# Optimization experiments

Hardware: AMD Instinct MI355X
Metric: run time of the kernel (lower is better)

## Reference

```python
import jax, jax.numpy as jnp
import numpy as np

B, H, W, C = 32, 56, 56, 192
WS, SS, NH = 7, 3, 6  # window, shift, heads
N = WS * WS
HIDDEN = int(C * 4.0)
TABLE = (2 * WS - 1) * (2 * WS - 1)  # 169
EPS = 1e-5

# Relative position index, faithful to the source (meshgrid default 'xy',
# and the source multiplies BOTH coord channels by (2*ws-1), so indices can
# exceed the table size; gather uses clip like jnp.take's jit behavior).
_coords = np.stack(np.meshgrid(np.arange(WS), np.arange(WS))).reshape(2, -1)
_rel = (_coords[:, :, None] - _coords[:, None, :]).transpose(1, 2, 0)
_rel = (_rel + WS - 1) * (2 * WS - 1)
REL_IDX = jnp.asarray(_rel.sum(-1))  # [N, N]

# Shift attention mask (static), labels regions then marks cross-region pairs.
_m = np.zeros((H, W))
_cnt = 0
for hs in [slice(0, -WS), slice(-WS, -SS), slice(-SS, None)]:
    for ws_ in [slice(0, -WS), slice(-WS, -SS), slice(-SS, None)]:
        _m[hs, ws_] = _cnt
        _cnt += 1
_mw = _m.reshape(H // WS, WS, W // WS, WS).transpose(0, 2, 1, 3).reshape(-1, N)
ATTN_MASK = jnp.asarray((_mw[:, None, :] != _mw[:, :, None]).astype(np.float32))  # [nW, N, N]
NW = ATTN_MASK.shape[0]


def layer_norm(x, g, b):
    mu = jnp.mean(x, axis=-1, keepdims=True)
    xc = x - mu
    var = jnp.mean(xc * xc, axis=-1, keepdims=True)
    return xc * jax.lax.rsqrt(var + EPS) * g + b


def window_partition(x):  # [B,H,W,C] -> [B*nW, N, C]
    x = x.reshape(B, H // WS, WS, W // WS, WS, C).transpose(0, 1, 3, 2, 4, 5)
    return x.reshape(-1, N, C)


def window_reverse(w):  # [B*nW, N, C] -> [B,H,W,C]
    x = w.reshape(B, H // WS, W // WS, WS, WS, C).transpose(0, 1, 3, 2, 4, 5)
    return x.reshape(B, H, W, C)


def setup_inputs() -> dict:
    key = jax.random.key(0)
    ks = jax.random.split(key, 16)
    s = lambda fan_in: 1.0 / np.sqrt(fan_in)
    return {
        "x": jax.random.normal(ks[0], (B, H * W, C), jnp.float32),
        "norm1_g": jnp.ones((C,), jnp.float32),
        "norm1_b": jnp.zeros((C,), jnp.float32),
        "qkv_w": jax.random.normal(ks[1], (C, 3 * C), jnp.float32) * s(C),
        "qkv_b": jnp.zeros((3 * C,), jnp.float32),
        "rel_table": jax.random.normal(ks[2], (TABLE, NH), jnp.float32) * 0.02,
        "proj_w": jax.random.normal(ks[3], (C, C), jnp.float32) * s(C),
        "proj_b": jnp.zeros((C,), jnp.float32),
        "norm2_g": jnp.ones((C,), jnp.float32),
        "norm2_b": jnp.zeros((C,), jnp.float32),
        "fc1_w": jax.random.normal(ks[4], (C, HIDDEN), jnp.float32) * s(C),
        "fc1_b": jnp.zeros((HIDDEN,), jnp.float32),
        "fc2_w": jax.random.normal(ks[5], (HIDDEN, C), jnp.float32) * s(HIDDEN),
        "fc2_b": jnp.zeros((C,), jnp.float32),
    }


def reference(x, norm1_g, norm1_b, qkv_w, qkv_b, rel_table, proj_w, proj_b,
              norm2_g, norm2_b, fc1_w, fc1_b, fc2_w, fc2_b):
    shortcut = x
    h = layer_norm(x, norm1_g, norm1_b).reshape(B, H, W, C)
    # cyclic shift
    h = jnp.roll(h, shift=(-SS, -SS), axis=(1, 2))
    xw = window_partition(h)  # [B*nW, N, C]

    # window attention
    qkv = xw @ qkv_w + qkv_b  # [B*nW, N, 3C]
    q, k, v = jnp.split(qkv, 3, axis=-1)
    hd = C // NH
    q = q.reshape(-1, N, NH, hd).transpose(0, 2, 1, 3) * (hd ** -0.5)
    k = k.reshape(-1, N, NH, hd).transpose(0, 2, 1, 3)
    v = v.reshape(-1, N, NH, hd).transpose(0, 2, 1, 3)
    attn = jnp.einsum("whnd,whmd->whnm", q, k)  # [B*nW, NH, N, N]
    bias = jnp.take(rel_table, REL_IDX, axis=0, mode="clip")  # [N,N,NH]
    attn = attn + bias.transpose(2, 0, 1)[None]
    attn = attn.reshape(B, NW, NH, N, N) + ATTN_MASK[None, :, None] * -100.0
    attn = jax.nn.softmax(attn.reshape(-1, NH, N, N), axis=-1)
    o = jnp.einsum("whnm,whmd->whnd", attn, v)
    o = o.transpose(0, 2, 1, 3).reshape(-1, N, C)
    o = o @ proj_w + proj_b

    h = window_reverse(o)
    h = jnp.roll(h, shift=(SS, SS), axis=(1, 2)).reshape(B, H * W, C)
    x = shortcut + h
    # MLP
    m = layer_norm(x, norm2_g, norm2_b)
    m = jax.nn.gelu(m @ fc1_w + fc1_b, approximate=False) @ fc2_w + fc2_b
    return x + m
```

## Files before the change

### kernel.cpp

```cpp
#include <hip/hip_runtime.h>
#include <hip/hip_bf16.h>


using f32x4  = __attribute__((ext_vector_type(4))) float;
using short8 = __attribute__((ext_vector_type(8))) short;
typedef unsigned short ushort_t;

__device__ __forceinline__ ushort_t f2bf(float f) {
    __hip_bfloat16 h = __float2bfloat16(f);
    return __builtin_bit_cast(ushort_t, h);
}
__device__ __forceinline__ f32x4 mfma16(short8 a, short8 b, f32x4 c) {
    return __builtin_amdgcn_mfma_f32_16x16x32_bf16(a, b, c, 0, 0, 0);
}
__device__ __forceinline__ float fast_gelu(float h) {
    float hh = h * h;
    float p  = __builtin_fmaf(hh, 0.044715f, 1.0f);
    float z  = h * (-1.5957691216057308f);
    float em = __expf(p * z);
    return h * __builtin_amdgcn_rcpf(1.0f + em);
}

#define CC 192

#define OFF_QKVT   0
#define OFF_PROJT  221184
#define OFF_FC1T   294912
#define OFF_FC2T   589824
#define OFF_BIAS   884736
#define OFF_MASK   942592
#define OFF_BMT    1557504
#define OFF_QG     7848960
#define OFF_KG     46384128
#define OFF_VG     84919296
#define WS_NEED    123454464
#define PREP_SMALL 610438
#define PREP_BIG   2183302

__global__ void prep_kernel(const float* __restrict__ qkv_w, const float* __restrict__ proj_w,
                            const float* __restrict__ fc1_w, const float* __restrict__ fc2_w,
                            const float* __restrict__ rel_table,
                            ushort_t* __restrict__ qkvT, ushort_t* __restrict__ projT,
                            ushort_t* __restrict__ fc1T, ushort_t* __restrict__ fc2T,
                            float* __restrict__ biasT, float* __restrict__ maskT,
                            float* __restrict__ bmT, int full) {
    int idx = blockIdx.x * 256 + threadIdx.x;
    if (idx < 110592) { int n = idx / 192, k = idx % 192; qkvT[idx] = f2bf(qkv_w[k * 576 + n]); return; }
    idx -= 110592;
    if (idx < 36864) { int n = idx / 192, k = idx % 192; projT[idx] = f2bf(proj_w[k * 192 + n]); return; }
    idx -= 36864;
    if (idx < 147456) { int n = idx / 192, k = idx % 192; fc1T[idx] = f2bf(fc1_w[k * 768 + n]); return; }
    idx -= 147456;
    if (idx < 147456) { int n = idx / 768, k = idx % 768; fc2T[idx] = f2bf(fc2_w[k * 192 + n]); return; }
    idx -= 147456;
    if (idx < 14406) {
        int h = idx / 2401; int rest = idx % 2401; int a = rest / 49, b = rest % 49;
        int d = 13 * ((a % 7) - (b % 7) + (a / 7) - (b / 7) + 12);
        if (d > 168) d = 168;
        biasT[idx] = rel_table[d * 6 + h];
        return;
    }
    idx -= 14406;
    if (idx < 153664) {
        int w = idx / 2401; int rest = idx % 2401; int a = rest / 49, b = rest % 49;
        int wy = w / 8, wx = w % 8;
        int ya = wy * 7 + a / 7, xa = wx * 7 + a % 7;
        int yb = wy * 7 + b / 7, xb = wx * 7 + b % 7;
        int lya = ya < 49 ? 0 : (ya < 53 ? 1 : 2);
        int lxa = xa < 49 ? 0 : (xa < 53 ? 1 : 2);
        int lyb = yb < 49 ? 0 : (yb < 53 ? 1 : 2);
        int lxb = xb < 49 ? 0 : (xb < 53 ? 1 : 2);
        maskT[idx] = ((lya * 3 + lxa) != (lyb * 3 + lxb)) ? -100.0f : 0.0f;
        return;
    }
    idx -= 153664;
    if (full && idx < 1572864) {
        int wi = idx / 24576; int r2 = idx % 24576;
        int h = r2 / 4096; int r3 = r2 % 4096;
        int col = r3 / 64, row = r3 % 64;
        float v = -1e30f;
        if (row < 49 && col < 49) {
            int d = 13 * ((row % 7) - (col % 7) + (row / 7) - (col / 7) + 12);
            if (d > 168) d = 168;
            float bias = rel_table[d * 6 + h];
            int wy = wi / 8, wx = wi % 8;
            int ya = wy * 7 + row / 7, xa = wx * 7 + row % 7;
            int yb = wy * 7 + col / 7, xb = wx * 7 + col % 7;
            int lya = ya < 49 ? 0 : (ya < 53 ? 1 : 2);
            int lxa = xa < 49 ? 0 : (xa < 53 ? 1 : 2);
            int lyb = yb < 49 ? 0 : (yb < 53 ? 1 : 2);
            int lxb = xb < 49 ? 0 : (xb < 53 ? 1 : 2);
            float mask = ((lya * 3 + lxa) != (lyb * 3 + lxb)) ? -100.0f : 0.0f;
            v = bias + mask;
        }
        bmT[idx] = v;
        return;
    }
}

__global__ __launch_bounds__(256, 3) void lnqkv_kernel(
    const float* __restrict__ x, const float* __restrict__ n1g, const float* __restrict__ n1b,
    const ushort_t* __restrict__ qkvT, const float* __restrict__ qkv_b,
    ushort_t* __restrict__ qg, ushort_t* __restrict__ kg, ushort_t* __restrict__ vg) {
    __shared__ ushort_t xln [64 * 200];
    __shared__ ushort_t qkvs[64 * 200];
    const int tid = threadIdx.x;
    const int wave = tid >> 6, lane = tid & 63;
    const int ln16 = lane & 15, sub = lane >> 4;
    const int t0 = blockIdx.x * 64;
    const f32x4 zero4 = {0.f, 0.f, 0.f, 0.f};

    {
        float g0 = n1g[lane], g1 = n1g[lane + 64], g2 = n1g[lane + 128];
        float bb0 = n1b[lane], bb1 = n1b[lane + 64], bb2 = n1b[lane + 128];
        for (int rb = 0; rb < 4; ++rb) {
            int row0 = wave * 16 + rb * 4;
            float v0[4], v1[4], v2[4], s[4], q[4];
            #pragma unroll
            for (int j = 0; j < 4; ++j) {
                const float* xr = x + (size_t)(t0 + row0 + j) * CC;
                v0[j] = xr[lane]; v1[j] = xr[lane + 64]; v2[j] = xr[lane + 128];
            }
            #pragma unroll
            for (int j = 0; j < 4; ++j) {
                s[j] = v0[j] + v1[j] + v2[j];
                q[j] = v0[j] * v0[j] + v1[j] * v1[j] + v2[j] * v2[j];
            }
            #pragma unroll
            for (int m = 32; m; m >>= 1) {
                #pragma unroll
                for (int j = 0; j < 4; ++j) { s[j] += __shfl_xor(s[j], m); q[j] += __shfl_xor(q[j], m); }
            }
            #pragma unroll
            for (int j = 0; j < 4; ++j) {
                float mu = s[j] * (1.0f / 192.0f);
                float var = q[j] * (1.0f / 192.0f) - mu * mu;
                float rs = rsqrtf(var + 1e-5f);
                int row = row0 + j;
                xln[row * 200 + lane]       = f2bf((v0[j] - mu) * rs * g0 + bb0);
                xln[row * 200 + lane + 64]  = f2bf((v1[j] - mu) * rs * g1 + bb1);
                xln[row * 200 + lane + 128] = f2bf((v2[j] - mu) * rs * g2 + bb2);
            }
        }
    }
    __syncthreads();

    ushort_t* dsts[3] = {qg, kg, vg};
    for (int v = 0; v < 3; ++v) {
        f32x4 acc[4][3];
        #pragma unroll
        for (int m = 0; m < 4; ++m)
            #pragma unroll
            for (int n = 0; n < 3; ++n) acc[m][n] = zero4;
        for (int kk = 0; kk < 6; ++kk) {
            short8 a[4];
            #pragma unroll
            for (int m = 0; m < 4; ++m)
                a[m] = *(const short8*)(xln + (m * 16 + ln16) * 200 + kk * 32 + 8 * sub);
            #pragma unroll
            for (int n = 0; n < 3; ++n) {
                short8 b = *(const short8*)(qkvT + (size_t)(v * 192 + (wave * 3 + n) * 16 + ln16) * 192 + kk * 32 + 8 * sub);
                #pragma unroll
                for (int m = 0; m < 4; ++m) acc[m][n] = mfma16(a[m], b, acc[m][n]);
            }
        }
        #pragma unroll
        for (int n = 0; n < 3; ++n) {
            int col = (wave * 3 + n) * 16 + ln16;
            float bv = qkv_b[v * 192 + col];
            #pragma unroll
            for (int m = 0; m < 4; ++m)
                #pragma unroll
                for (int r = 0; r < 4; ++r) {
                    int row = m * 16 + 4 * sub + r;
                    float val = acc[m][n][r] + bv;
                    if (v == 0) val *= 0.17677669529663689f;
                    qkvs[row * 200 + col] = f2bf(val);
                }
        }
        __syncthreads();
        ushort_t* dst = dsts[v];
        for (int i = tid; i < 1536; i += 256) {
            int row = i / 24, c = i % 24;
            short8 vv = *(const short8*)(qkvs + row * 200 + c * 8);
            *(short8*)(dst + (size_t)(t0 + row) * 192 + c * 8) = vv;
        }
        __syncthreads();
    }
}

__global__ __launch_bounds__(256, 3) void attnmlp_kernel(
    const float* __restrict__ x, const float* __restrict__ proj_b,
    const ushort_t* __restrict__ qg, const ushort_t* __restrict__ kg,
    const ushort_t* __restrict__ vg, const ushort_t* __restrict__ projT,
    const float* __restrict__ bmT,
    const float* __restrict__ n2g, const float* __restrict__ n2b,
    const float* __restrict__ fc1_b, const float* __restrict__ fc2_b,
    const ushort_t* __restrict__ fc1T, const ushort_t* __restrict__ fc2T,
    float* __restrict__ out) {
    __shared__ __align__(16) char smem[51200];
    ushort_t* vt   = (ushort_t*)smem;
    ushort_t* PO   = (ushort_t*)(smem + 27648);
    ushort_t* aln  = (ushort_t*)smem;
    ushort_t* hidc = (ushort_t*)(smem + 25600);
    float*    fout = (float*)smem;

    const int tid = threadIdx.x;
    const int wave = tid >> 6, lane = tid & 63;
    const int ln16 = lane & 15, sub = lane >> 4;
    const int win = blockIdx.x;
    const int b = win >> 6, wi = win & 63;
    const int wy = wi >> 3, wx = wi & 7;
    const f32x4 zero4 = {0.f, 0.f, 0.f, 0.f};

    size_t tokA;
    {
        int j = wave * 16 + ln16; if (j > 48) j = 48;
        int y  = wy * 7 + j / 7 + 3; if (y >= 56) y -= 56;
        int xx = wx * 7 + j % 7 + 3; if (xx >= 56) xx -= 56;
        tokA = (size_t)(b * 3136 + y * 56 + xx);
    }
    size_t tokB[4];
    #pragma unroll
    for (int n = 0; n < 4; ++n) {
        int j = n * 16 + ln16; if (j > 48) j = 48;
        int y  = wy * 7 + j / 7 + 3; if (y >= 56) y -= 56;
        int xx = wx * 7 + j % 7 + 3; if (xx >= 56) xx -= 56;
        tokB[n] = (size_t)(b * 3136 + y * 56 + xx);
    }
    const float* bmw = bmT + (size_t)wi * 24576 + (size_t)(wave * 16 + 4 * sub);

    short8 qf = *(const short8*)(qg + tokA * 192 + 8 * sub);
    short8 kf[4];
    f32x4  bv[4];
    #pragma unroll
    for (int n = 0; n < 4; ++n) {
        kf[n] = *(const short8*)(kg + tokB[n] * 192 + 8 * sub);
        bv[n] = *(const f32x4*)(bmw + (n * 16 + ln16) * 64);
    }

    {
        int j = tid & 63;
        int jj = j < 49 ? j : 48;
        int y  = wy * 7 + jj / 7 + 3; if (y >= 56) y -= 56;
        int xx = wx * 7 + jj % 7 + 3; if (xx >= 56) xx -= 56;
        size_t tokV = (size_t)(b * 3136 + y * 56 + xx);
        const bool valid = j < 49;
        #pragma unroll
        for (int pass = 0; pass < 6; ++pass) {
            int c8 = pass * 32 + (tid >> 6) * 8;
            if (valid) {
                short8 vv = *(const short8*)(vg + tokV * 192 + c8);
                #pragma unroll
                for (int q = 0; q < 8; ++q) vt[(c8 + q) * 72 + j] = ((ushort_t*)&vv)[q];
            } else {
                #pragma unroll
                for (int q = 0; q < 8; ++q) vt[(c8 + q) * 72 + j] = 0;
            }
        }
    }

    f32x4 accP[12];
    #pragma unroll
    for (int n = 0; n < 12; ++n) accP[n] = zero4;
    ushort_t* Pw = PO + wave * (16 * 72);
    __syncthreads();

    #pragma unroll
    for (int h = 0; h < 6; ++h) {
        f32x4 s4[4];
        #pragma unroll
        for (int n = 0; n < 4; ++n) s4[n] = mfma16(qf, kf[n], zero4);
        short8 qn; short8 kn[4]; f32x4 bn[4];
        if (h < 5) {
            qn = *(const short8*)(qg + tokA * 192 + (h + 1) * 32 + 8 * sub);
            #pragma unroll
            for (int n = 0; n < 4; ++n) {
                kn[n] = *(const short8*)(kg + tokB[n] * 192 + (h + 1) * 32 + 8 * sub);
                bn[n] = *(const f32x4*)(bmw + (h + 1) * 4096 + (n * 16 + ln16) * 64);
            }
        }
        #pragma unroll
        for (int n = 0; n < 4; ++n)
            #pragma unroll
            for (int r = 0; r < 4; ++r) s4[n][r] += bv[n][r];
        #pragma unroll
        for (int r = 0; r < 4; ++r) {
            float mx = fmaxf(fmaxf(s4[0][r], s4[1][r]), fmaxf(s4[2][r], s4[3][r]));
            mx = fmaxf(mx, __shfl_xor(mx, 1, 16));
            mx = fmaxf(mx, __shfl_xor(mx, 2, 16));
            mx = fmaxf(mx, __shfl_xor(mx, 4, 16));
            mx = fmaxf(mx, __shfl_xor(mx, 8, 16));
            float e0 = __expf(s4[0][r] - mx), e1 = __expf(s4[1][r] - mx);
            float e2 = __expf(s4[2][r] - mx), e3 = __expf(s4[3][r] - mx);
            float sm = e0 + e1 + e2 + e3;
            sm += __shfl_xor(sm, 1, 16);
            sm += __shfl_xor(sm, 2, 16);
            sm += __shfl_xor(sm, 4, 16);
            sm += __shfl_xor(sm, 8, 16);
            float inv = 1.0f / sm;
            int rl = 4 * sub + r;
            Pw[rl * 72 +      ln16] = f2bf(e0 * inv);
            Pw[rl * 72 + 16 + ln16] = f2bf(e1 * inv);
            Pw[rl * 72 + 32 + ln16] = f2bf(e2 * inv);
            Pw[rl * 72 + 48 + ln16] = f2bf(e3 * inv);
        }
        short8 ap0 = *(const short8*)(Pw + ln16 * 72 + 8 * sub);
        short8 ap1 = *(const short8*)(Pw + ln16 * 72 + 32 + 8 * sub);
        f32x4 o2[2]; o2[0] = zero4; o2[1] = zero4;
        #pragma unroll
        for (int n2 = 0; n2 < 2; ++n2) {
            short8 bv0 = *(const short8*)(vt + (h * 32 + n2 * 16 + ln16) * 72 + 8 * sub);
            short8 bv1 = *(const short8*)(vt + (h * 32 + n2 * 16 + ln16) * 72 + 32 + 8 * sub);
            o2[n2] = mfma16(ap0, bv0, o2[n2]);
            o2[n2] = mfma16(ap1, bv1, o2[n2]);
        }
        #pragma unroll
        for (int n2 = 0; n2 < 2; ++n2)
            #pragma unroll
            for (int r = 0; r < 4; ++r)
                Pw[(4 * sub + r) * 72 + n2 * 16 + ln16] = f2bf(o2[n2][r]);
        {
            short8 ao = *(const short8*)(Pw + ln16 * 72 + 8 * sub);
            #pragma unroll
            for (int n = 0; n < 12; ++n) {
                short8 bp = *(const short8*)(projT + (size_t)(n * 16 + ln16) * 192 + h * 32 + 8 * sub);
                accP[n] = mfma16(ao, bp, accP[n]);
            }
        }
        if (h < 5) {
            qf = qn;
            #pragma unroll
            for (int n = 0; n < 4; ++n) { kf[n] = kn[n]; bv[n] = bn[n]; }
        }
    }

    #pragma unroll
    for (int n = 0; n < 12; ++n) {
        int col = n * 16 + ln16;
        float pb = proj_b[col];
        #pragma unroll
        for (int r = 0; r < 4; ++r) {
            int row = wave * 16 + 4 * sub + r;
            float v = accP[n][r] + pb;
            if (row < 49) {
                int y  = wy * 7 + row / 7 + 3; if (y >= 56) y -= 56;
                int xx = wx * 7 + row % 7 + 3; if (xx >= 56) xx -= 56;
                size_t g = (size_t)(b * 3136 + y * 56 + xx) * CC;
                v += x[g + col];
                out[g + col] = v;
            }
            accP[n][r] = v;
        }
    }
    __threadfence_block();

    float mu4[4], rs4[4];
    {
        float s[4], qs[4];
        #pragma unroll
        for (int r = 0; r < 4; ++r) { s[r] = 0.f; qs[r] = 0.f; }
        #pragma unroll
        for (int n = 0; n < 12; ++n)
            #pragma unroll
            for (int r = 0; r < 4; ++r) {
                float v = accP[n][r];
                s[r] += v; qs[r] += v * v;
            }
        #pragma unroll
        for (int m = 1; m < 16; m <<= 1) {
            #pragma unroll
            for (int r = 0; r < 4; ++r) {
                s[r]  += __shfl_xor(s[r],  m, 16);
                qs[r] += __shfl_xor(qs[r], m, 16);
            }
        }
        #pragma unroll
        for (int r = 0; r < 4; ++r) {
            float mu = s[r] * (1.0f / 192.0f);
            float var = qs[r] * (1.0f / 192.0f) - mu * mu;
            mu4[r] = mu;
            rs4[r] = rsqrtf(var + 1e-5f);
        }
    }
    __syncthreads();

    short8 b1p[3];
    #pragma unroll
    for (int n = 0; n < 3; ++n)
        b1p[n] = *(const short8*)(fc1T + (size_t)(wave * 48 + n * 16 + ln16) * 192 + 8 * sub);

    #pragma unroll
    for (int n = 0; n < 12; ++n) {
        int col = n * 16 + ln16;
        float g = n2g[col], bb = n2b[col];
        #pragma unroll
        for (int r = 0; r < 4; ++r) {
            int row = wave * 16 + 4 * sub + r;
            aln[row * 200 + col] = f2bf((accP[n][r] - mu4[r]) * rs4[r] * g + bb);
        }
    }
    __syncthreads();

    f32x4 accO[4][3];
    #pragma unroll
    for (int m = 0; m < 4; ++m)
        #pragma unroll
        for (int n = 0; n < 3; ++n) accO[m][n] = zero4;

    for (int c = 0; c < 4; ++c) {
        f32x4 acc1[4][3];
        #pragma unroll
        for (int m = 0; m < 4; ++m)
            #pragma unroll
            for (int n = 0; n < 3; ++n) acc1[m][n] = zero4;
        #pragma unroll
        for (int kk = 0; kk < 6; ++kk) {
            short8 a[4];
            #pragma unroll
            for (int m = 0; m < 4; ++m)
                a[m] = *(const short8*)(aln + (m * 16 + ln16) * 200 + kk * 32 + 8 * sub);
            short8 bb[3];
            if (kk == 0) {
                bb[0] = b1p[0]; bb[1] = b1p[1]; bb[2] = b1p[2];
            } else {
                #pragma unroll
                for (int n = 0; n < 3; ++n)
                    bb[n] = *(const short8*)(fc1T + (size_t)(c * 192 + wave * 48 + n * 16 + ln16) * 192 + kk * 32 + 8 * sub);
            }
            __builtin_amdgcn_s_setprio(1);
            #pragma unroll
            for (int n = 0; n < 3; ++n)
                #pragma unroll
                for (int m = 0; m < 4; ++m) acc1[m][n] = mfma16(a[m], bb[n], acc1[m][n]);
            __builtin_amdgcn_s_setprio(0);
        }
        short8 b2p[3];
        #pragma unroll
        for (int n = 0; n < 3; ++n)
            b2p[n] = *(const short8*)(fc2T + (size_t)(wave * 48 + n * 16 + ln16) * 768 + c * 192 + 8 * sub);
        if (c < 3) {
            #pragma unroll
            for (int n = 0; n < 3; ++n)
                b1p[n] = *(const short8*)(fc1T + (size_t)((c + 1) * 192 + wave * 48 + n * 16 + ln16) * 192 + 8 * sub);
        }
        #pragma unroll
        for (int n = 0; n < 3; ++n) {
            int cl = wave * 48 + n * 16 + ln16;
            float fb = fc1_b[c * 192 + cl];
            #pragma unroll
            for (int m = 0; m < 4; ++m)
                #pragma unroll
                for (int r = 0; r < 4; ++r) {
                    float hv = acc1[m][n][r] + fb;
                    hidc[(m * 16 + 4 * sub + r) * 200 + cl] = f2bf(fast_gelu(hv));
                }
        }
        __syncthreads();
        #pragma unroll
        for (int kk = 0; kk < 6; ++kk) {
            short8 a[4];
            #pragma unroll
            for (int m = 0; m < 4; ++m)
                a[m] = *(const short8*)(hidc + (m * 16 + ln16) * 200 + kk * 32 + 8 * sub);
            short8 bb[3];
            if (kk == 0) {
                bb[0] = b2p[0]; bb[1] = b2p[1]; bb[2] = b2p[2];
            } else {
                #pragma unroll
                for (int n = 0; n < 3; ++n)
                    bb[n] = *(const short8*)(fc2T + (size_t)(wave * 48 + n * 16 + ln16) * 768 + c * 192 + kk * 32 + 8 * sub);
            }
            __builtin_amdgcn_s_setprio(1);
            #pragma unroll
            for (int n = 0; n < 3; ++n)
                #pragma unroll
                for (int m = 0; m < 4; ++m) accO[m][n] = mfma16(a[m], bb[n], accO[m][n]);
            __builtin_amdgcn_s_setprio(0);
        }
        __syncthreads();
    }

    #pragma unroll
    for (int n = 0; n < 3; ++n) {
        int col = wave * 48 + n * 16 + ln16;
        float fb = fc2_b[col];
        #pragma unroll
        for (int m = 0; m < 4; ++m)
            #pragma unroll
            for (int r = 0; r < 4; ++r)
                fout[(m * 16 + 4 * sub + r) * 196 + col] = accO[m][n][r] + fb;
    }
    __syncthreads();
    for (int i = tid; i < 2352; i += 256) {
        int row = i / 48, c4 = (i % 48) * 4;
        int y  = wy * 7 + row / 7 + 3; if (y >= 56) y -= 56;
        int xx = wx * 7 + row % 7 + 3; if (xx >= 56) xx -= 56;
        float* op = out + (size_t)(b * 3136 + y * 56 + xx) * CC + c4;
        f32x4 sv = *(const f32x4*)(fout + row * 196 + c4);
        f32x4 ov = *(const f32x4*)op;
        #pragma unroll
        for (int q = 0; q < 4; ++q) ov[q] += sv[q];
        *(f32x4*)op = ov;
    }
}

__global__ __launch_bounds__(256, 3) void attn_kernel(
    const float* __restrict__ x, const float* __restrict__ n1g, const float* __restrict__ n1b,
    const float* __restrict__ qkv_b, const float* __restrict__ proj_b,
    const ushort_t* __restrict__ qkvT, const ushort_t* __restrict__ projT,
    const float* __restrict__ biasT, const float* __restrict__ maskT,
    float* __restrict__ out) {
    __shared__ ushort_t xln[64 * 200];
    __shared__ ushort_t qo [64 * 40];
    __shared__ ushort_t kl [64 * 40];
    __shared__ ushort_t vt [32 * 72];
    __shared__ ushort_t Pl [64 * 72];
    const int tid = threadIdx.x;
    const int wave = tid >> 6, lane = tid & 63;
    const int ln16 = lane & 15, sub = lane >> 4;
    const int w = blockIdx.x;
    const int batch = w >> 6, wi = w & 63;
    const int wy = wi >> 3, wx = wi & 7;
    const f32x4 zero4 = {0.f, 0.f, 0.f, 0.f};

    for (int rr = 0; rr < 16; ++rr) {
        int row = wave * 16 + rr;
        if (row < 49) {
            int ty = row / 7, tx = row % 7;
            int y  = wy * 7 + ty + 3; if (y >= 56) y -= 56;
            int xx = wx * 7 + tx + 3; if (xx >= 56) xx -= 56;
            const float* xr = x + (size_t)(batch * 3136 + y * 56 + xx) * CC;
            float v0 = xr[lane], v1 = xr[lane + 64], v2 = xr[lane + 128];
            float s = v0 + v1 + v2;
            #pragma unroll
            for (int m = 32; m; m >>= 1) s += __shfl_xor(s, m);
            float mu = s * (1.0f / 192.0f);
            float d0 = v0 - mu, d1 = v1 - mu, d2 = v2 - mu;
            float q = d0 * d0 + d1 * d1 + d2 * d2;
            #pragma unroll
            for (int m = 32; m; m >>= 1) q += __shfl_xor(q, m);
            float rs = rsqrtf(q * (1.0f / 192.0f) + 1e-5f);
            xln[row * 200 + lane]       = f2bf(d0 * rs * n1g[lane]       + n1b[lane]);
            xln[row * 200 + lane + 64]  = f2bf(d1 * rs * n1g[lane + 64]  + n1b[lane + 64]);
            xln[row * 200 + lane + 128] = f2bf(d2 * rs * n1g[lane + 128] + n1b[lane + 128]);
        } else {
            xln[row * 200 + lane] = 0; xln[row * 200 + lane + 64] = 0; xln[row * 200 + lane + 128] = 0;
        }
    }

    f32x4 accP[12];
    #pragma unroll
    for (int n = 0; n < 12; ++n) accP[n] = zero4;
    const float scale = 0.17677669529663689f;
    const float* mptr = maskT + wi * 2401;

    for (int h = 0; h < 6; ++h) {
        f32x4 acc6[6];
        #pragma unroll
        for (int n = 0; n < 6; ++n) acc6[n] = zero4;
        const int cb0 = h * 32;
        for (int kk = 0; kk < 6; ++kk) {
            short8 a = *(const short8*)(xln + (wave * 16 + ln16) * 200 + kk * 32 + 8 * sub);
            #pragma unroll
            for (int n = 0; n < 6; ++n) {
                int colbase = (n >> 1) * 192 + cb0 + (n & 1) * 16;
                short8 b = *(const short8*)(qkvT + (size_t)(colbase + ln16) * 192 + kk * 32 + 8 * sub);
                acc6[n] = mfma16(a, b, acc6[n]);
            }
        }
        #pragma unroll
        for (int n = 0; n < 6; ++n) {
            int colbase = (n >> 1) * 192 + cb0 + (n & 1) * 16;
            float bv = qkv_b[colbase + ln16];
            int dim = (n & 1) * 16 + ln16;
            #pragma unroll
            for (int r = 0; r < 4; ++r) {
                int row = wave * 16 + 4 * sub + r;
                ushort_t hv = f2bf(acc6[n][r] + bv);
                if (n < 2)      qo[row * 40 + dim] = hv;
                else if (n < 4) kl[row * 40 + dim] = hv;
                else            vt[dim * 72 + row] = hv;
            }
        }
        __syncthreads();

        f32x4 s4[4];
        {
            short8 aq = *(const short8*)(qo + (wave * 16 + ln16) * 40 + 8 * sub);
            #pragma unroll
            for (int n = 0; n < 4; ++n) {
                short8 bk = *(const short8*)(kl + (n * 16 + ln16) * 40 + 8 * sub);
                s4[n] = mfma16(aq, bk, zero4);
            }
        }
        const float* bptr = biasT + h * 2401;
        #pragma unroll
        for (int n = 0; n < 4; ++n) {
            int col = n * 16 + ln16;
            #pragma unroll
            for (int r = 0; r < 4; ++r) {
                int row = wave * 16 + 4 * sub + r;
                s4[n][r] = (row < 49 && col < 49)
                    ? s4[n][r] * scale + bptr[row * 49 + col] + mptr[row * 49 + col]
                    : -1e30f;
            }
        }
        #pragma unroll
        for (int r = 0; r < 4; ++r) {
            float mx = fmaxf(fmaxf(s4[0][r], s4[1][r]), fmaxf(s4[2][r], s4[3][r]));
            mx = fmaxf(mx, __shfl_xor(mx, 1, 16));
            mx = fmaxf(mx, __shfl_xor(mx, 2, 16));
            mx = fmaxf(mx, __shfl_xor(mx, 4, 16));
            mx = fmaxf(mx, __shfl_xor(mx, 8, 16));
            float e0 = __expf(s4[0][r] - mx), e1 = __expf(s4[1][r] - mx);
            float e2 = __expf(s4[2][r] - mx), e3 = __expf(s4[3][r] - mx);
            float sm = e0 + e1 + e2 + e3;
            sm += __shfl_xor(sm, 1, 16);
            sm += __shfl_xor(sm, 2, 16);
            sm += __shfl_xor(sm, 4, 16);
            sm += __shfl_xor(sm, 8, 16);
            float inv = 1.0f / sm;
            int row = wave * 16 + 4 * sub + r;
            Pl[row * 72 +      ln16] = f2bf(e0 * inv);
            Pl[row * 72 + 16 + ln16] = f2bf(e1 * inv);
            Pl[row * 72 + 32 + ln16] = f2bf(e2 * inv);
            Pl[row * 72 + 48 + ln16] = f2bf(e3 * inv);
        }
        f32x4 o2[2]; o2[0] = zero4; o2[1] = zero4;
        #pragma unroll
        for (int ks = 0; ks < 2; ++ks) {
            short8 ap = *(const short8*)(Pl + (wave * 16 + ln16) * 72 + ks * 32 + 8 * sub);
            #pragma unroll
            for (int n2 = 0; n2 < 2; ++n2) {
                short8 bv = *(const short8*)(vt + (n2 * 16 + ln16) * 72 + ks * 32 + 8 * sub);
                o2[n2] = mfma16(ap, bv, o2[n2]);
            }
        }
        #pragma unroll
        for (int n2 = 0; n2 < 2; ++n2)
            #pragma unroll
            for (int r = 0; r < 4; ++r) {
                int row = wave * 16 + 4 * sub + r;
                qo[row * 40 + n2 * 16 + ln16] = f2bf(o2[n2][r]);
            }
        {
            short8 ao = *(const short8*)(qo + (wave * 16 + ln16) * 40 + 8 * sub);
            #pragma unroll
            for (int n = 0; n < 12; ++n) {
                short8 bp = *(const short8*)(projT + (size_t)(n * 16 + ln16) * 192 + h * 32 + 8 * sub);
                accP[n] = mfma16(ao, bp, accP[n]);
            }
        }
        __syncthreads();
    }

    #pragma unroll
    for (int n = 0; n < 12; ++n) {
        int col = n * 16 + ln16;
        float pb = proj_b[col];
        #pragma unroll
        for (int r = 0; r < 4; ++r) {
            int row = wave * 16 + 4 * sub + r;
            if (row < 49) {
                int ty = row / 7, tx = row % 7;
                int y  = wy * 7 + ty + 3; if (y >= 56) y -= 56;
                int xx = wx * 7 + tx + 3; if (xx >= 56) xx -= 56;
                size_t g = (size_t)(batch * 3136 + y * 56 + xx) * CC;
                out[g + col] = accP[n][r] + pb + x[g + col];
            }
        }
    }
}

__global__ __launch_bounds__(256, 3) void mlp5_kernel(
    float* __restrict__ out, const float* __restrict__ n2g, const float* __restrict__ n2b,
    const float* __restrict__ fc1_b, const float* __restrict__ fc2_b,
    const ushort_t* __restrict__ fc1T, const ushort_t* __restrict__ fc2T) {
    __shared__ ushort_t smem[2][64 * 200];
    ushort_t* aln  = smem[0];
    ushort_t* hidc = smem[1];
    float* fout = (float*)&smem[0][0];
    const int tid = threadIdx.x;
    const int wave = tid >> 6, lane = tid & 63;
    const int ln16 = lane & 15, sub = lane >> 4;
    const size_t t0 = (size_t)blockIdx.x * 64;
    const f32x4 zero4 = {0.f, 0.f, 0.f, 0.f};

    short8 b1p[3];
    #pragma unroll
    for (int n = 0; n < 3; ++n)
        b1p[n] = *(const short8*)(fc1T + (size_t)(wave * 48 + n * 16 + ln16) * 192 + 8 * sub);

    {
        float g0 = n2g[lane], g1 = n2g[lane + 64], g2 = n2g[lane + 128];
        float bb0 = n2b[lane], bb1 = n2b[lane + 64], bb2 = n2b[lane + 128];
        for (int rb = 0; rb < 4; ++rb) {
            int row0 = wave * 16 + rb * 4;
            float v0[4], v1[4], v2[4], s[4], q[4];
            #pragma unroll
            for (int j = 0; j < 4; ++j) {
                const float* xr = out + (t0 + row0 + j) * CC;
                v0[j] = xr[lane]; v1[j] = xr[lane + 64]; v2[j] = xr[lane + 128];
            }
            #pragma unroll
            for (int j = 0; j < 4; ++j) {
                s[j] = v0[j] + v1[j] + v2[j];
                q[j] = v0[j] * v0[j] + v1[j] * v1[j] + v2[j] * v2[j];
            }
            #pragma unroll
            for (int m = 32; m; m >>= 1) {
                #pragma unroll
                for (int j = 0; j < 4; ++j) { s[j] += __shfl_xor(s[j], m); q[j] += __shfl_xor(q[j], m); }
            }
            #pragma unroll
            for (int j = 0; j < 4; ++j) {
                float mu = s[j] * (1.0f / 192.0f);
                float var = q[j] * (1.0f / 192.0f) - mu * mu;
                float rs = rsqrtf(var + 1e-5f);
                int row = row0 + j;
                aln[row * 200 + lane]       = f2bf((v0[j] - mu) * rs * g0 + bb0);
                aln[row * 200 + lane + 64]  = f2bf((v1[j] - mu) * rs * g1 + bb1);
                aln[row * 200 + lane + 128] = f2bf((v2[j] - mu) * rs * g2 + bb2);
            }
        }
    }
    __syncthreads();

    f32x4 accO[4][3];
    #pragma unroll
    for (int m = 0; m < 4; ++m)
        #pragma unroll
        for (int n = 0; n < 3; ++n) accO[m][n] = zero4;

    for (int c = 0; c < 4; ++c) {
        f32x4 acc1[4][3];
        #pragma unroll
        for (int m = 0; m < 4; ++m)
            #pragma unroll
            for (int n = 0; n < 3; ++n) acc1[m][n] = zero4;
        #pragma unroll
        for (int kk = 0; kk < 6; ++kk) {
            short8 a[4];
            #pragma unroll
            for (int m = 0; m < 4; ++m)
                a[m] = *(const short8*)(aln + (m * 16 + ln16) * 200 + kk * 32 + 8 * sub);
            short8 bb[3];
            if (kk == 0) {
                bb[0] = b1p[0]; bb[1] = b1p[1]; bb[2] = b1p[2];
            } else {
                #pragma unroll
                for (int n = 0; n < 3; ++n)
                    bb[n] = *(const short8*)(fc1T + (size_t)(c * 192 + wave * 48 + n * 16 + ln16) * 192 + kk * 32 + 8 * sub);
            }
            __builtin_amdgcn_s_setprio(1);
            #pragma unroll
            for (int n = 0; n < 3; ++n)
                #pragma unroll
                for (int m = 0; m < 4; ++m) acc1[m][n] = mfma16(a[m], bb[n], acc1[m][n]);
            __builtin_amdgcn_s_setprio(0);
        }
        short8 b2p[3];
        #pragma unroll
        for (int n = 0; n < 3; ++n)
            b2p[n] = *(const short8*)(fc2T + (size_t)(wave * 48 + n * 16 + ln16) * 768 + c * 192 + 8 * sub);
        if (c < 3) {
            #pragma unroll
            for (int n = 0; n < 3; ++n)
                b1p[n] = *(const short8*)(fc1T + (size_t)((c + 1) * 192 + wave * 48 + n * 16 + ln16) * 192 + 8 * sub);
        }
        #pragma unroll
        for (int n = 0; n < 3; ++n) {
            int cl = wave * 48 + n * 16 + ln16;
            float fb = fc1_b[c * 192 + cl];
            #pragma unroll
            for (int m = 0; m < 4; ++m)
                #pragma unroll
                for (int r = 0; r < 4; ++r) {
                    float hv = acc1[m][n][r] + fb;
                    hidc[(m * 16 + 4 * sub + r) * 200 + cl] = f2bf(fast_gelu(hv));
                }
        }
        __syncthreads();
        #pragma unroll
        for (int kk = 0; kk < 6; ++kk) {
            short8 a[4];
            #pragma unroll
            for (int m = 0; m < 4; ++m)
                a[m] = *(const short8*)(hidc + (m * 16 + ln16) * 200 + kk * 32 + 8 * sub);
            short8 bb[3];
            if (kk == 0) {
                bb[0] = b2p[0]; bb[1] = b2p[1]; bb[2] = b2p[2];
            } else {
                #pragma unroll
                for (int n = 0; n < 3; ++n)
                    bb[n] = *(const short8*)(fc2T + (size_t)(wave * 48 + n * 16 + ln16) * 768 + c * 192 + kk * 32 + 8 * sub);
            }
            __builtin_amdgcn_s_setprio(1);
            #pragma unroll
            for (int n = 0; n < 3; ++n)
                #pragma unroll
                for (int m = 0; m < 4; ++m) accO[m][n] = mfma16(a[m], bb[n], accO[m][n]);
            __builtin_amdgcn_s_setprio(0);
        }
        __syncthreads();
    }

    #pragma unroll
    for (int n = 0; n < 3; ++n) {
        int col = wave * 48 + n * 16 + ln16;
        float fb = fc2_b[col];
        #pragma unroll
        for (int m = 0; m < 4; ++m)
            #pragma unroll
            for (int r = 0; r < 4; ++r)
                fout[(m * 16 + 4 * sub + r) * 196 + col] = accO[m][n][r] + fb;
    }
    __syncthreads();
    for (int i = tid; i < 3072; i += 256) {
        int row = i / 48, c4 = (i % 48) * 4;
        f32x4 sv = *(const f32x4*)(fout + row * 196 + c4);
        float* op = out + (t0 + row) * CC + c4;
        f32x4 ov = *(const f32x4*)op;
        #pragma unroll
        for (int q = 0; q < 4; ++q) ov[q] += sv[q];
        *(f32x4*)op = ov;
    }
}

extern "C" void kernel_launch(void* const* d_in, const int* in_sizes, int n_in,
                              void* d_out, int out_size, void* d_ws, size_t ws_size,
                              hipStream_t stream) {
    const float* x      = (const float*)d_in[0];
    const float* n1g    = (const float*)d_in[1];
    const float* n1b    = (const float*)d_in[2];
    const float* qkv_w  = (const float*)d_in[3];
    const float* qkv_b  = (const float*)d_in[4];
    const float* rel_t  = (const float*)d_in[5];
    const float* proj_w = (const float*)d_in[6];
    const float* proj_b = (const float*)d_in[7];
    const float* n2g    = (const float*)d_in[8];
    const float* n2b    = (const float*)d_in[9];
    const float* fc1_w  = (const float*)d_in[10];
    const float* fc1_b  = (const float*)d_in[11];
    const float* fc2_w  = (const float*)d_in[12];
    const float* fc2_b  = (const float*)d_in[13];
    float* out = (float*)d_out;

    char* ws = (char*)d_ws;
    ushort_t* qkvT  = (ushort_t*)(ws + OFF_QKVT);
    ushort_t* projT = (ushort_t*)(ws + OFF_PROJT);
    ushort_t* fc1T  = (ushort_t*)(ws + OFF_FC1T);
    ushort_t* fc2T  = (ushort_t*)(ws + OFF_FC2T);
    float* biasT    = (float*)(ws + OFF_BIAS);
    float* maskT    = (float*)(ws + OFF_MASK);
    float* bmT      = (float*)(ws + OFF_BMT);
    ushort_t* qg    = (ushort_t*)(ws + OFF_QG);
    ushort_t* kg    = (ushort_t*)(ws + OFF_KG);
    ushort_t* vg    = (ushort_t*)(ws + OFF_VG);

    const int big = ws_size >= (size_t)WS_NEED;
    const int prep_total = big ? PREP_BIG : PREP_SMALL;
    prep_kernel<<<(prep_total + 255) / 256, 256, 0, stream>>>(
        qkv_w, proj_w, fc1_w, fc2_w, rel_t, qkvT, projT, fc1T, fc2T, biasT, maskT, bmT, big);

    if (big) {
        lnqkv_kernel<<<1568, 256, 0, stream>>>(x, n1g, n1b, qkvT, qkv_b, qg, kg, vg);
        attnmlp_kernel<<<2048, 256, 0, stream>>>(x, proj_b, qg, kg, vg, projT, bmT,
                                                 n2g, n2b, fc1_b, fc2_b, fc1T, fc2T, out);
    } else {
        attn_kernel<<<2048, 256, 0, stream>>>(x, n1g, n1b, qkv_b, proj_b,
                                              qkvT, projT, biasT, maskT, out);
        mlp5_kernel<<<1568, 256, 0, stream>>>(out, n2g, n2b, fc1_b, fc2_b, fc1T, fc2T);
    }
}
```

Measured before the change: 436.5 us.

## Prefetch residual, drop softmax max subtraction, defer normalization, add MFMA priority hints

Loads the residual x values into registers before the attention loop so the epilogue no longer waits on global reads. Softmax skips the row-max reduction and exponentiates the raw scores, then applies 1/sum to the P·V output instead of to every probability. MFMA sections are wrapped in s_setprio to favour matrix issue. Skipping the max relies on scores staying small enough not to overflow exp, and holding 48 extra floats per thread raises register pressure.

```diff
diff --git a/kernel.cpp b/kernel.cpp
--- a/kernel.cpp
+++ b/kernel.cpp
@@ -239,6 +239,17 @@
         bv[n] = *(const f32x4*)(bmw + (n * 16 + ln16) * 64);
     }
 
+    float xres[12][4];
+    #pragma unroll
+    for (int r = 0; r < 4; ++r) {
+        int row = wave * 16 + 4 * sub + r; if (row > 48) row = 48;
+        int y  = wy * 7 + row / 7 + 3; if (y >= 56) y -= 56;
+        int xx = wx * 7 + row % 7 + 3; if (xx >= 56) xx -= 56;
+        const float* xr = x + (size_t)(b * 3136 + y * 56 + xx) * CC + ln16;
+        #pragma unroll
+        for (int n = 0; n < 12; ++n) xres[n][r] = xr[n * 16];
+    }
+
     {
         int j = tid & 63;
         int jj = j < 49 ? j : 48;
@@ -269,8 +280,10 @@
     #pragma unroll
     for (int h = 0; h < 6; ++h) {
         f32x4 s4[4];
+        __builtin_amdgcn_s_setprio(1);
         #pragma unroll
         for (int n = 0; n < 4; ++n) s4[n] = mfma16(qf, kf[n], zero4);
+        __builtin_amdgcn_s_setprio(0);
         short8 qn; short8 kn[4]; f32x4 bn[4];
         if (h < 5) {
             qn = *(const short8*)(qg + tokA * 192 + (h + 1) * 32 + 8 * sub);
@@ -284,30 +297,27 @@
         for (int n = 0; n < 4; ++n)
             #pragma unroll
             for (int r = 0; r < 4; ++r) s4[n][r] += bv[n][r];
+        float inv[4];
         #pragma unroll
         for (int r = 0; r < 4; ++r) {
-            float mx = fmaxf(fmaxf(s4[0][r], s4[1][r]), fmaxf(s4[2][r], s4[3][r]));
-            mx = fmaxf(mx, __shfl_xor(mx, 1, 16));
-            mx = fmaxf(mx, __shfl_xor(mx, 2, 16));
-            mx = fmaxf(mx, __shfl_xor(mx, 4, 16));
-            mx = fmaxf(mx, __shfl_xor(mx, 8, 16));
-            float e0 = __expf(s4[0][r] - mx), e1 = __expf(s4[1][r] - mx);
-            float e2 = __expf(s4[2][r] - mx), e3 = __expf(s4[3][r] - mx);
+            float e0 = __expf(s4[0][r]), e1 = __expf(s4[1][r]);
+            float e2 = __expf(s4[2][r]), e3 = __expf(s4[3][r]);
+            int rl = 4 * sub + r;
+            Pw[rl * 72 +      ln16] = f2bf(e0);
+            Pw[rl * 72 + 16 + ln16] = f2bf(e1);
+            Pw[rl * 72 + 32 + ln16] = f2bf(e2);
+            Pw[rl * 72 + 48 + ln16] = f2bf(e3);
             float sm = e0 + e1 + e2 + e3;
             sm += __shfl_xor(sm, 1, 16);
             sm += __shfl_xor(sm, 2, 16);
             sm += __shfl_xor(sm, 4, 16);
             sm += __shfl_xor(sm, 8, 16);
-            float inv = 1.0f / sm;
-            int rl = 4 * sub + r;
-            Pw[rl * 72 +      ln16] = f2bf(e0 * inv);
-            Pw[rl * 72 + 16 + ln16] = f2bf(e1 * inv);
-            Pw[rl * 72 + 32 + ln16] = f2bf(e2 * inv);
-            Pw[rl * 72 + 48 + ln16] = f2bf(e3 * inv);
+            inv[r] = 1.0f / sm;
         }
         short8 ap0 = *(const short8*)(Pw + ln16 * 72 + 8 * sub);
         short8 ap1 = *(const short8*)(Pw + ln16 * 72 + 32 + 8 * sub);
         f32x4 o2[2]; o2[0] = zero4; o2[1] = zero4;
+        __builtin_amdgcn_s_setprio(1);
         #pragma unroll
         for (int n2 = 0; n2 < 2; ++n2) {
             short8 bv0 = *(const short8*)(vt + (h * 32 + n2 * 16 + ln16) * 72 + 8 * sub);
@@ -315,18 +325,21 @@
             o2[n2] = mfma16(ap0, bv0, o2[n2]);
             o2[n2] = mfma16(ap1, bv1, o2[n2]);
         }
+        __builtin_amdgcn_s_setprio(0);
         #pragma unroll
         for (int n2 = 0; n2 < 2; ++n2)
             #pragma unroll
             for (int r = 0; r < 4; ++r)
-                Pw[(4 * sub + r) * 72 + n2 * 16 + ln16] = f2bf(o2[n2][r]);
+                Pw[(4 * sub + r) * 72 + n2 * 16 + ln16] = f2bf(o2[n2][r] * inv[r]);
         {
             short8 ao = *(const short8*)(Pw + ln16 * 72 + 8 * sub);
+            __builtin_amdgcn_s_setprio(1);
             #pragma unroll
             for (int n = 0; n < 12; ++n) {
                 short8 bp = *(const short8*)(projT + (size_t)(n * 16 + ln16) * 192 + h * 32 + 8 * sub);
                 accP[n] = mfma16(ao, bp, accP[n]);
             }
+            __builtin_amdgcn_s_setprio(0);
         }
         if (h < 5) {
             qf = qn;
@@ -342,13 +355,11 @@
         #pragma unroll
         for (int r = 0; r < 4; ++r) {
             int row = wave * 16 + 4 * sub + r;
-            float v = accP[n][r] + pb;
+            float v = accP[n][r] + pb + xres[n][r];
             if (row < 49) {
                 int y  = wy * 7 + row / 7 + 3; if (y >= 56) y -= 56;
                 int xx = wx * 7 + row % 7 + 3; if (xx >= 56) xx -= 56;
-                size_t g = (size_t)(b * 3136 + y * 56 + xx) * CC;
-                v += x[g + col];
-                out[g + col] = v;
+                out[(size_t)(b * 3136 + y * 56 + xx) * CC + col] = v;
             }
             accP[n][r] = v;
         }
```

Measured after the change: 561.8 us. 1.29x slower.
